# Kernel optimization log

Measured on AMD Instinct MI355X. Metric: run time of the kernel, lower is better.

The kernel has to match this reference:

```python
import jax, jax.numpy as jnp
import numpy as np

D_MODEL = 1024
D_INNER = 2048  # expand * d_model
D_STATE = 16
D_CONV = 4
DT_RANK = 64    # ceil(d_model / 16)
B_SZ, L_SEQ = 2, 1024


def setup_inputs() -> dict:
    key = jax.random.key(0)
    ks = jax.random.split(key, 8)
    s = lambda fan_in: 1.0 / np.sqrt(fan_in)
    x = jax.random.normal(ks[0], (B_SZ, L_SEQ, D_MODEL), dtype=jnp.float32)
    in_proj_w = jax.random.normal(ks[1], (2 * D_INNER, D_MODEL), jnp.float32) * s(D_MODEL)
    conv_w = jax.random.normal(ks[2], (D_INNER, 1, D_CONV), jnp.float32) * s(D_CONV)
    conv_b = jax.random.normal(ks[3], (D_INNER,), jnp.float32) * 0.02
    x_proj_w = jax.random.normal(ks[4], (DT_RANK + 2 * D_STATE, D_INNER), jnp.float32) * s(D_INNER)
    dt_proj_w = jax.random.normal(ks[5], (D_INNER, DT_RANK), jnp.float32) * s(DT_RANK)
    dt_proj_b = jax.random.normal(ks[6], (D_INNER,), jnp.float32) * 0.02
    A_log = jnp.broadcast_to(jnp.log(jnp.arange(1, D_STATE + 1, dtype=jnp.float32)), (D_INNER, D_STATE))
    D_param = jnp.ones((D_INNER,), jnp.float32)
    out_proj_w = jax.random.normal(ks[7], (D_MODEL, D_INNER), jnp.float32) * s(D_INNER)
    return dict(x=x, in_proj_w=in_proj_w, conv_w=conv_w, conv_b=conv_b,
                x_proj_w=x_proj_w, dt_proj_w=dt_proj_w, dt_proj_b=dt_proj_b,
                A_log=A_log, D_param=D_param, out_proj_w=out_proj_w)


def _mamba_forward(x, in_proj_w, conv_w, conv_b, x_proj_w, dt_proj_w, dt_proj_b, A_log, D_param, out_proj_w):
    B, L, _ = x.shape
    # in_proj: (B,L,2*d_inner) -> split into conv branch and gate
    xz = jnp.einsum('bld,ed->ble', x, in_proj_w)
    x_br, z = jnp.split(xz, 2, axis=-1)
    # depthwise causal conv1d (left pad d_conv-1, truncate to L == torch pad+slice)
    xc = jnp.transpose(x_br, (0, 2, 1))  # (B, d_inner, L)
    xc = jax.lax.conv_general_dilated(
        xc, conv_w, window_strides=(1,), padding=[(D_CONV - 1, 0)],
        dimension_numbers=('NCH', 'OIH', 'NCH'), feature_group_count=D_INNER)
    xc = xc + conv_b[None, :, None]
    u = jax.nn.silu(jnp.transpose(xc, (0, 2, 1)))  # (B, L, d_inner) = SSM input
    # input-dependent params
    proj = jnp.einsum('bld,ed->ble', u, x_proj_w)
    delta_raw, B_in, C_in = jnp.split(proj, [DT_RANK, DT_RANK + D_STATE], axis=-1)
    delta = jax.nn.softplus(jnp.einsum('blr,dr->bld', delta_raw, dt_proj_w) + dt_proj_b)
    A = -jnp.exp(A_log)  # (d_inner, d_state)

    def step(h, inp):
        d_t, b_t, c_t, u_t = inp  # (B,d_inner),(B,d_state),(B,d_state),(B,d_inner)
        dA = jnp.exp(d_t[:, :, None] * A)                       # (B,d_inner,d_state)
        h = dA * h + (d_t * u_t)[:, :, None] * b_t[:, None, :]  # ZOH-ish update
        y_t = jnp.einsum('bds,bs->bd', h, c_t) + D_param * u_t
        return h, y_t

    h0 = jnp.zeros((B, D_INNER, D_STATE), dtype=x.dtype)
    inputs = (jnp.swapaxes(delta, 0, 1), jnp.swapaxes(B_in, 0, 1),
              jnp.swapaxes(C_in, 0, 1), jnp.swapaxes(u, 0, 1))
    _, ys = jax.lax.scan(step, h0, inputs)  # (L, B, d_inner)
    y = jnp.swapaxes(ys, 0, 1) * jax.nn.silu(z)
    return jnp.einsum('ble,de->bld', y, out_proj_w)


def reference(x, in_proj_w, conv_w, conv_b, x_proj_w, dt_proj_w, dt_proj_b, A_log, D_param, out_proj_w):
    return _mamba_forward(x, in_proj_w, conv_w, conv_b, x_proj_w, dt_proj_w, dt_proj_b, A_log, D_param, out_proj_w)
```

## Files before the change

kernel.cpp:

```cpp
#include <hip/hip_runtime.h>
#include <hip/hip_bf16.h>

#define D_MODEL 1024
#define D_INNER 2048
#define D_STATE 16
#define D_CONV  4
#define DT_RANK 64
#define B_SZ    2
#define L_SEQ   1024
#define BL      (B_SZ * L_SEQ)
#define NPROJ   (DT_RANK + 2 * D_STATE)

typedef __attribute__((ext_vector_type(8))) short bf16x8;
typedef __attribute__((ext_vector_type(4))) float floatx4;
typedef unsigned short ushort_t;

__device__ __forceinline__ void mfma_bf16(floatx4& acc, bf16x8 a, bf16x8 b) {
    asm volatile("v_mfma_f32_16x16x32_bf16 %0, %1, %2, %0"
                 : "+v"(acc) : "v"(a), "v"(b));
}

__device__ __forceinline__ void cvt_hilo(float f, ushort_t& hi, ushort_t& lo) {
    __hip_bfloat16 h = __float2bfloat16(f);
    hi = *(ushort_t*)&h;
    __hip_bfloat16 l = __float2bfloat16(f - __bfloat162float(h));
    lo = *(ushort_t*)&l;
}

__device__ __forceinline__ void cvt_store4(float4 v, ushort_t* hi, ushort_t* lo) {
    ushort4 h, l;
    cvt_hilo(v.x, h.x, l.x);
    cvt_hilo(v.y, h.y, l.y);
    cvt_hilo(v.z, h.z, l.z);
    cvt_hilo(v.w, h.w, l.w);
    *(ushort4*)hi = h;
    *(ushort4*)lo = l;
}

#define N4_WI 1048576
#define N4_WO 524288
#define N4_X  524288
#define N4_TOT  (N4_WI + N4_WO + N4_X)

__global__ __launch_bounds__(256) void cvt_static(
    const float* __restrict__ wi, ushort_t* wihi, ushort_t* wilo,
    const float* __restrict__ wo, ushort_t* wohi, ushort_t* wolo,
    const float* __restrict__ x,  ushort_t* xhi,  ushort_t* xlo)
{
    int i = blockIdx.x * 256 + threadIdx.x;
    if (i >= N4_TOT) return;
    const float* src; ushort_t *dh, *dl;
    if (i < N4_WI)                 { src = wi; dh = wihi; dl = wilo; }
    else if ((i -= N4_WI) < N4_WO) { src = wo; dh = wohi; dl = wolo; }
    else                           { i -= N4_WO; src = x; dh = xhi; dl = xlo; }
    float4 v = ((const float4*)src)[i];
    cvt_store4(v, dh + i * 4, dl + i * 4);
}

template <int TM, int TN, int KSPLIT>
__global__ __launch_bounds__(256, 2) void gemm_pre(
    const ushort_t* __restrict__ Ahi, const ushort_t* __restrict__ Alo, int lda,
    const ushort_t* __restrict__ Bhi, const ushort_t* __restrict__ Blo, int ldb,
    float* __restrict__ C, int ldc, int K, size_t cslice)
{
    constexpr int LDT = 32;
    constexpr int IT = TM / 32, JT = TN / 32;
    __shared__ __align__(16) ushort_t As[2][TM * LDT];
    __shared__ __align__(16) ushort_t Bs[2][TN * LDT];

    const int tid = threadIdx.x;
    const int bm = blockIdx.y * TM;
    const int bn = blockIdx.x * TN;
    const int kstart = (KSPLIT > 1) ? blockIdx.z * (K / KSPLIT) : 0;
    const int kend   = (KSPLIT > 1) ? kstart + K / KSPLIT : K;

    const int wave = tid >> 6;
    const int lane = tid & 63;
    const int wm = (wave >> 1) * (TM / 2);
    const int wn = (wave & 1) * (TN / 2);
    const int ml = lane & 15;
    const int q  = lane >> 4;

    floatx4 acc[IT][JT];
#pragma unroll
    for (int i = 0; i < IT; ++i)
#pragma unroll
        for (int j = 0; j < JT; ++j) acc[i][j] = (floatx4)0.f;

    for (int k0 = kstart; k0 < kend; k0 += 32) {
        __syncthreads();
#pragma unroll
        for (int ci = 0; ci < TM / 64; ++ci) {
            const int flat = tid + 256 * ci;
            const int r = flat >> 2, c = flat & 3;
            const int p = (c ^ ((r >> 1) & 3)) * 8;
            *(uint4*)&As[0][r * LDT + p] =
                *(const uint4*)(Ahi + (size_t)(bm + r) * lda + k0 + c * 8);
            *(uint4*)&As[1][r * LDT + p] =
                *(const uint4*)(Alo + (size_t)(bm + r) * lda + k0 + c * 8);
        }
#pragma unroll
        for (int ci = 0; ci < TN / 64; ++ci) {
            const int flat = tid + 256 * ci;
            const int r = flat >> 2, c = flat & 3;
            const int p = (c ^ ((r >> 1) & 3)) * 8;
            *(uint4*)&Bs[0][r * LDT + p] =
                *(const uint4*)(Bhi + (size_t)(bn + r) * ldb + k0 + c * 8);
            *(uint4*)&Bs[1][r * LDT + p] =
                *(const uint4*)(Blo + (size_t)(bn + r) * ldb + k0 + c * 8);
        }
        __syncthreads();

        bf16x8 ah[IT], al[IT], bh[JT], bl[JT];
#pragma unroll
        for (int i = 0; i < IT; ++i) {
            const int r = wm + i * 16 + ml;
            const int p = (q ^ ((r >> 1) & 3)) * 8;
            ah[i] = *(const bf16x8*)&As[0][r * LDT + p];
            al[i] = *(const bf16x8*)&As[1][r * LDT + p];
        }
#pragma unroll
        for (int j = 0; j < JT; ++j) {
            const int r = wn + j * 16 + ml;
            const int p = (q ^ ((r >> 1) & 3)) * 8;
            bh[j] = *(const bf16x8*)&Bs[0][r * LDT + p];
            bl[j] = *(const bf16x8*)&Bs[1][r * LDT + p];
        }
#pragma unroll
        for (int i = 0; i < IT; ++i)
#pragma unroll
            for (int j = 0; j < JT; ++j) {
                mfma_bf16(acc[i][j], ah[i], bh[j]);
                mfma_bf16(acc[i][j], ah[i], bl[j]);
                mfma_bf16(acc[i][j], al[i], bh[j]);
            }
    }

    asm volatile("s_nop 7\n\ts_nop 7\n\ts_nop 7" ::: "memory");

    float* Cb = (KSPLIT > 1) ? C + (size_t)blockIdx.z * cslice : C;
#pragma unroll
    for (int i = 0; i < IT; ++i)
#pragma unroll
        for (int j = 0; j < JT; ++j)
#pragma unroll
            for (int r = 0; r < 4; ++r) {
                const int row = bm + wm + i * 16 + q * 4 + r;
                const int col = bn + wn + j * 16 + ml;
                Cb[(size_t)row * ldc + col] = acc[i][j][r];
            }
}

__global__ __launch_bounds__(256) void fold_out(
    const float* __restrict__ s, float* __restrict__ out)
{
    const int i = blockIdx.x * 256 + threadIdx.x;
    const float4* s4 = (const float4*)s;
    constexpr int SL = BL * D_MODEL / 4;
    float4 a = s4[i], b = s4[i + SL], c = s4[i + 2 * SL], d = s4[i + 3 * SL];
    ((float4*)out)[i] = make_float4(a.x + b.x + c.x + d.x,
                                    a.y + b.y + c.y + d.y,
                                    a.z + b.z + c.z + d.z,
                                    a.w + b.w + c.w + d.w);
}

__global__ __launch_bounds__(256) void fold_proj(
    const float* __restrict__ pp, float* __restrict__ proj)
{
    const int i = blockIdx.x * 256 + threadIdx.x;
    constexpr int SL = BL * NPROJ / 4;
    float4 acc = make_float4(0.f, 0.f, 0.f, 0.f);
#pragma unroll
    for (int sp = 0; sp < 16; ++sp) {
        float4 v = ((const float4*)pp)[i + sp * SL];
        acc.x += v.x; acc.y += v.y; acc.z += v.z; acc.w += v.w;
    }
    ((float4*)proj)[i] = acc;
}

__global__ __launch_bounds__(256) void delta_kernel(
    const float* __restrict__ proj,
    const float* __restrict__ Wd,
    const float* __restrict__ bias,
    float* __restrict__ xz)
{
    __shared__ float ps[16][65];
    const int d  = blockIdx.x * 256 + threadIdx.x;
    const int r0 = blockIdx.y * 16;

    {
        const int rr = threadIdx.x >> 4;
        const int cc = (threadIdx.x & 15) * 4;
        float4 v = *(const float4*)(proj + (size_t)(r0 + rr) * NPROJ + cc);
        ps[rr][cc + 0] = v.x; ps[rr][cc + 1] = v.y;
        ps[rr][cc + 2] = v.z; ps[rr][cc + 3] = v.w;
    }
    __syncthreads();

    float w[64];
#pragma unroll
    for (int c4 = 0; c4 < 16; ++c4) {
        float4 v = *(const float4*)(Wd + (size_t)d * 64 + c4 * 4);
        w[c4 * 4 + 0] = v.x; w[c4 * 4 + 1] = v.y;
        w[c4 * 4 + 2] = v.z; w[c4 * 4 + 3] = v.w;
    }
    const float bv = bias[d];

#pragma unroll
    for (int rr = 0; rr < 16; ++rr) {
        float acc = bv;
#pragma unroll
        for (int k = 0; k < 64; ++k) acc += ps[rr][k] * w[k];
        acc = (acc > 20.f) ? acc : log1pf(__expf(acc));
        xz[(size_t)(r0 + rr) * 4096 + d] = acc;
    }
}

#define PKC 128
#define PSC 64

__global__ __launch_bounds__(256) void gemm_proj_conv(
    const float* __restrict__ xz,
    const float* __restrict__ conv_w,
    const float* __restrict__ conv_b,
    const float* __restrict__ Wp,
    float* __restrict__ projp,
    float* __restrict__ u_out)
{
    __shared__ float us[PSC][65];
    __shared__ float wsh[PSC][100];

    const int tid = threadIdx.x;
    const int bm = blockIdx.y * 64;
    const int kbase0 = blockIdx.x * PKC;

    const int tx = tid & 15;
    const int ty = tid >> 4;

    float acc[4][6];
#pragma unroll
    for (int i = 0; i < 4; ++i)
#pragma unroll
        for (int j = 0; j < 6; ++j) acc[i][j] = 0.f;

    for (int sc = 0; sc < PKC / PSC; ++sc) {
        const int kb = kbase0 + sc * PSC;
        __syncthreads();
#pragma unroll
        for (int i = 0; i < 4; ++i) {
            const int flat = tid + 256 * i;
            const int r  = flat >> 4;
            const int kk = (flat & 15) * 4;
            const int k  = kb + kk;
            const int rr = bm + r;
            const int t  = rr & (L_SEQ - 1);
            const float* base = xz + (size_t)rr * 4096 + k;
            float4 x0 = *(const float4*)(base);
            float4 x1 = (t >= 1) ? *(const float4*)(base - 4096)  : make_float4(0,0,0,0);
            float4 x2 = (t >= 2) ? *(const float4*)(base - 8192)  : make_float4(0,0,0,0);
            float4 x3 = (t >= 3) ? *(const float4*)(base - 12288) : make_float4(0,0,0,0);
            float4 cb = *(const float4*)(conv_b + k);
            float4 w0 = ((const float4*)conv_w)[k + 0];
            float4 w1 = ((const float4*)conv_w)[k + 1];
            float4 w2 = ((const float4*)conv_w)[k + 2];
            float4 w3 = ((const float4*)conv_w)[k + 3];
            float4 uo;
            { float a = cb.x + w0.x*x3.x + w0.y*x2.x + w0.z*x1.x + w0.w*x0.x;
              uo.x = a / (1.f + __expf(-a)); }
            { float a = cb.y + w1.x*x3.y + w1.y*x2.y + w1.z*x1.y + w1.w*x0.y;
              uo.y = a / (1.f + __expf(-a)); }
            { float a = cb.z + w2.x*x3.z + w2.y*x2.z + w2.z*x1.z + w2.w*x0.z;
              uo.z = a / (1.f + __expf(-a)); }
            { float a = cb.w + w3.x*x3.w + w3.y*x2.w + w3.z*x1.w + w3.w*x0.w;
              uo.w = a / (1.f + __expf(-a)); }
            us[kk + 0][r] = uo.x;
            us[kk + 1][r] = uo.y;
            us[kk + 2][r] = uo.z;
            us[kk + 3][r] = uo.w;
            *(float4*)(u_out + (size_t)rr * D_INNER + k) = uo;
        }
#pragma unroll
        for (int i = 0; i < 6; ++i) {
            const int flat = tid + 256 * i;
            const int r = flat >> 4;
            const int k4 = flat & 15;
            float4 v = *(const float4*)(Wp + (size_t)r * D_INNER + kb + k4 * 4);
            wsh[k4*4+0][r] = v.x; wsh[k4*4+1][r] = v.y;
            wsh[k4*4+2][r] = v.z; wsh[k4*4+3][r] = v.w;
        }
        __syncthreads();

#pragma unroll 8
        for (int kk = 0; kk < PSC; ++kk) {
            float a[4], b[6];
#pragma unroll
            for (int i = 0; i < 4; ++i) a[i] = us[kk][ty * 4 + i];
#pragma unroll
            for (int j = 0; j < 6; ++j) b[j] = wsh[kk][tx + 16 * j];
#pragma unroll
            for (int i = 0; i < 4; ++i)
#pragma unroll
                for (int j = 0; j < 6; ++j) acc[i][j] += a[i] * b[j];
        }
    }

    float* pb = projp + (size_t)blockIdx.x * (BL * NPROJ);
#pragma unroll
    for (int i = 0; i < 4; ++i)
#pragma unroll
        for (int j = 0; j < 6; ++j)
            pb[(size_t)(bm + ty * 4 + i) * NPROJ + tx + 16 * j] = acc[i][j];
}

template <int CSv>
__global__ __launch_bounds__(256) void scan_phase_a(
    const float* __restrict__ xz,
    const float* __restrict__ u,
    const float* __restrict__ proj,
    const float* __restrict__ A_log,
    float* __restrict__ hloc,
    float* __restrict__ sumd,
    int nc)
{
    const int d = blockIdx.x * 256 + threadIdx.x;
    const int c = blockIdx.y;
    const int b = blockIdx.z;

    float a[D_STATE];
#pragma unroll
    for (int s = 0; s < D_STATE; ++s) a[s] = -__expf(A_log[d * D_STATE + s]);

    float h[D_STATE];
#pragma unroll
    for (int s = 0; s < D_STATE; ++s) h[s] = 0.f;
    float sd = 0.f;

    for (int t = c * CSv; t < (c + 1) * CSv; ++t) {
        const size_t bt = (size_t)b * L_SEQ + t;
        const float dv = xz[bt * (2 * D_INNER) + d];
        const float uv = u[bt * D_INNER + d];
        const float du = dv * uv;
        sd += dv;
        const float* pr = proj + bt * NPROJ;
#pragma unroll
        for (int s = 0; s < D_STATE; ++s)
            h[s] = __expf(dv * a[s]) * h[s] + du * pr[DT_RANK + s];
    }

    const size_t base = ((size_t)(b * nc + c) * D_STATE) * D_INNER + d;
#pragma unroll
    for (int s = 0; s < D_STATE; ++s) hloc[base + (size_t)s * D_INNER] = h[s];
    sumd[(size_t)(b * nc + c) * D_INNER + d] = sd;
}

__global__ __launch_bounds__(256) void scan_phase_b(
    const float* __restrict__ hloc,
    const float* __restrict__ sumd,
    const float* __restrict__ A_log,
    float* __restrict__ carry,
    int nc)
{
    const int g = blockIdx.x * 256 + threadIdx.x;
    const int d = g & (D_INNER - 1);
    const int s = (g >> 11) & (D_STATE - 1);
    const int b = g >> 15;

    const float a_s = -__expf(A_log[d * D_STATE + s]);

    float hc = 0.f;
    carry[((size_t)(b * nc + 0) * D_STATE + s) * D_INNER + d] = 0.f;

    for (int c = 1; c < nc; ++c) {
        const float sd = sumd[(size_t)(b * nc + c - 1) * D_INNER + d];
        const float hl = hloc[((size_t)(b * nc + c - 1) * D_STATE + s) * D_INNER + d];
        hc = __expf(a_s * sd) * hc + hl;
        carry[((size_t)(b * nc + c) * D_STATE + s) * D_INNER + d] = hc;
    }
}

template <int CSv>
__global__ __launch_bounds__(256) void scan_phase_c(
    const float* __restrict__ xz,
    const float* __restrict__ u,
    const float* __restrict__ proj,
    const float* __restrict__ A_log,
    const float* __restrict__ D_param,
    const float* __restrict__ carry,
    ushort_t* __restrict__ Yhi,
    ushort_t* __restrict__ Ylo,
    int nc)
{
    const int d = blockIdx.x * 256 + threadIdx.x;
    const int c = blockIdx.y;
    const int b = blockIdx.z;

    float a[D_STATE];
#pragma unroll
    for (int s = 0; s < D_STATE; ++s) a[s] = -__expf(A_log[d * D_STATE + s]);
    const float Dp = D_param[d];

    float h[D_STATE];
    const size_t cbase = ((size_t)(b * nc + c) * D_STATE) * D_INNER + d;
#pragma unroll
    for (int s = 0; s < D_STATE; ++s) h[s] = carry[cbase + (size_t)s * D_INNER];

    for (int t = c * CSv; t < (c + 1) * CSv; ++t) {
        const size_t bt = (size_t)b * L_SEQ + t;
        const float dv = xz[bt * (2 * D_INNER) + d];
        const float uv = u[bt * D_INNER + d];
        const float du = dv * uv;
        const float* pr = proj + bt * NPROJ;

        float acc = 0.f;
#pragma unroll
        for (int s = 0; s < D_STATE; ++s) {
            h[s] = __expf(dv * a[s]) * h[s] + du * pr[DT_RANK + s];
            acc += h[s] * pr[DT_RANK + D_STATE + s];
        }
        const float yv = acc + Dp * uv;

        const float zv = xz[bt * (2 * D_INNER) + D_INNER + d];
        const float gate = zv / (1.f + __expf(-zv));
        ushort_t hh, ll;
        cvt_hilo(yv * gate, hh, ll);
        Yhi[bt * D_INNER + d] = hh;
        Ylo[bt * D_INNER + d] = ll;
    }
}

extern "C" void kernel_launch(void* const* d_in, const int* in_sizes, int n_in,
                              void* d_out, int out_size, void* d_ws, size_t ws_size,
                              hipStream_t stream)
{
    const float* x         = (const float*)d_in[0];
    const float* in_proj_w = (const float*)d_in[1];
    const float* conv_w    = (const float*)d_in[2];
    const float* conv_b    = (const float*)d_in[3];
    const float* x_proj_w  = (const float*)d_in[4];
    const float* dt_proj_w = (const float*)d_in[5];
    const float* dt_proj_b = (const float*)d_in[6];
    const float* A_log     = (const float*)d_in[7];
    const float* D_param   = (const float*)d_in[8];
    const float* out_proj_w= (const float*)d_in[9];
    float* out = (float*)d_out;

    const size_t fixed =
        (size_t)BL * 4096 * 4 +
        (size_t)BL * 2048 * 4 +
        (size_t)BL * NPROJ * 4 +
        (size_t)(4096 + 2048) * 1024 * 2 * 2;
    const size_t need64 = fixed + (size_t)B_SZ * 64 * D_INNER * 4
                                + (size_t)B_SZ * 64 * D_STATE * D_INNER * 4;
    const int nc = (ws_size >= need64) ? 64 : 32;
    const int cs = L_SEQ / nc;

    float* xz    = (float*)d_ws;
    float* u     = xz    + (size_t)BL * 4096;
    float* proj  = u     + (size_t)BL * 2048;
    float* sumd  = proj  + (size_t)BL * NPROJ;
    float* carry = sumd  + (size_t)B_SZ * nc * D_INNER;
    ushort_t* Wihi = (ushort_t*)(carry + (size_t)B_SZ * nc * D_STATE * D_INNER);
    ushort_t* Wilo = Wihi + (size_t)4096 * 1024;
    ushort_t* Wohi = Wilo + (size_t)4096 * 1024;
    ushort_t* Wolo = Wohi + (size_t)1024 * 2048;
    ushort_t* Xhi  = (ushort_t*)carry;
    ushort_t* Xlo  = Xhi + (size_t)BL * D_MODEL;
    float*    hloc = (float*)Wihi;
    ushort_t* Yhi  = Wihi;
    ushort_t* Ylo  = Wilo;
    float*    projp = (float*)Wihi;
    float*    Cslc  = xz;

    dim3 blk(256);

    cvt_static<<<(N4_TOT + 255) / 256, blk, 0, stream>>>(
        in_proj_w, Wihi, Wilo, out_proj_w, Wohi, Wolo, x, Xhi, Xlo);

    gemm_pre<128, 128, 1><<<dim3(4096 / 128, BL / 128), blk, 0, stream>>>(
        Xhi, Xlo, D_MODEL, Wihi, Wilo, D_MODEL, xz, 2 * D_INNER, D_MODEL, 0);

    gemm_proj_conv<<<dim3(D_INNER / PKC, BL / 64), blk, 0, stream>>>(
        xz, conv_w, conv_b, x_proj_w, projp, u);

    fold_proj<<<(BL * NPROJ / 4) / 256, blk, 0, stream>>>(projp, proj);

    delta_kernel<<<dim3(D_INNER / 256, BL / 16), blk, 0, stream>>>(
        proj, dt_proj_w, dt_proj_b, xz);

    if (cs == 16) {
        scan_phase_a<16><<<dim3(D_INNER / 256, nc, B_SZ), blk, 0, stream>>>(
            xz, u, proj, A_log, hloc, sumd, nc);
    } else {
        scan_phase_a<32><<<dim3(D_INNER / 256, nc, B_SZ), blk, 0, stream>>>(
            xz, u, proj, A_log, hloc, sumd, nc);
    }
    scan_phase_b<<<dim3((B_SZ * D_INNER * D_STATE) / 256), blk, 0, stream>>>(
        hloc, sumd, A_log, carry, nc);
    if (cs == 16) {
        scan_phase_c<16><<<dim3(D_INNER / 256, nc, B_SZ), blk, 0, stream>>>(
            xz, u, proj, A_log, D_param, carry, Yhi, Ylo, nc);
    } else {
        scan_phase_c<32><<<dim3(D_INNER / 256, nc, B_SZ), blk, 0, stream>>>(
            xz, u, proj, A_log, D_param, carry, Yhi, Ylo, nc);
    }

    gemm_pre<128, 128, 4><<<dim3(D_MODEL / 128, BL / 128, 4), blk, 0, stream>>>(
        Yhi, Ylo, D_INNER, Wohi, Wolo, D_INNER, Cslc, D_MODEL, D_INNER,
        (size_t)BL * D_MODEL);
    fold_out<<<(BL * D_MODEL / 4) / 256, blk, 0, stream>>>(Cslc, out);
}
```

Measured before the change: 301.2 us.

## Double-buffer GEMM tiles using direct global-to-LDS loads per wave

The GEMM main loop now double-buffers its shared-memory tiles and fills them with global_load_lds, which copies straight from global memory into LDS without passing through registers. Each wave stages one of the four hi/lo A/B planes. The next K-tile is prefetched while the current one is multiplied, which drops one barrier per iteration and frees the registers that held staged data. In exchange LDS use doubles, which may cut occupancy, and the kernel is now restricted to 128x128 tiles. The direct-to-LDS path also relies on the row-swizzle lane mapping and on the 16-byte load size working correctly on this hardware.

```diff
diff --git a/kernel.cpp b/kernel.cpp
--- a/kernel.cpp
+++ b/kernel.cpp
@@ -63,10 +63,11 @@
     const ushort_t* __restrict__ Bhi, const ushort_t* __restrict__ Blo, int ldb,
     float* __restrict__ C, int ldc, int K, size_t cslice)
 {
+    static_assert(TM == 128 && TN == 128, "stage mapping assumes 128x128");
     constexpr int LDT = 32;
     constexpr int IT = TM / 32, JT = TN / 32;
-    __shared__ __align__(16) ushort_t As[2][TM * LDT];
-    __shared__ __align__(16) ushort_t Bs[2][TN * LDT];
+    __shared__ __align__(16) ushort_t As[2][2][TM * LDT];
+    __shared__ __align__(16) ushort_t Bs[2][2][TN * LDT];
 
     const int tid = threadIdx.x;
     const int bm = blockIdx.y * TM;
@@ -81,50 +82,57 @@
     const int ml = lane & 15;
     const int q  = lane >> 4;
 
+    const ushort_t* gplane = (wave == 0) ? Ahi : (wave == 1) ? Alo
+                           : (wave == 2) ? Bhi : Blo;
+    const int grow0 = (wave < 2) ? bm : bn;
+    const int gld   = (wave < 2) ? lda : ldb;
+    const int rsub  = lane >> 2;
+    const int gg    = ((lane & 3) ^ ((lane >> 3) & 3)) * 8;
+
+    auto stage = [&](int buf, int kc) {
+        ushort_t* lbase = (wave < 2) ? &As[buf][wave & 1][0]
+                                     : &Bs[buf][wave & 1][0];
+#pragma unroll
+        for (int u = 0; u < 8; ++u) {
+            const int R0 = u * 16;
+            const ushort_t* src =
+                gplane + (size_t)(grow0 + R0 + rsub) * gld + kc + gg;
+            __builtin_amdgcn_global_load_lds(
+                (const __attribute__((address_space(1))) unsigned int*)src,
+                (__attribute__((address_space(3))) unsigned int*)(lbase + R0 * LDT),
+                16, 0, 0);
+        }
+    };
+
     floatx4 acc[IT][JT];
 #pragma unroll
     for (int i = 0; i < IT; ++i)
 #pragma unroll
         for (int j = 0; j < JT; ++j) acc[i][j] = (floatx4)0.f;
 
-    for (int k0 = kstart; k0 < kend; k0 += 32) {
-        __syncthreads();
-#pragma unroll
-        for (int ci = 0; ci < TM / 64; ++ci) {
-            const int flat = tid + 256 * ci;
-            const int r = flat >> 2, c = flat & 3;
-            const int p = (c ^ ((r >> 1) & 3)) * 8;
-            *(uint4*)&As[0][r * LDT + p] =
-                *(const uint4*)(Ahi + (size_t)(bm + r) * lda + k0 + c * 8);
-            *(uint4*)&As[1][r * LDT + p] =
-                *(const uint4*)(Alo + (size_t)(bm + r) * lda + k0 + c * 8);
-        }
-#pragma unroll
-        for (int ci = 0; ci < TN / 64; ++ci) {
-            const int flat = tid + 256 * ci;
-            const int r = flat >> 2, c = flat & 3;
-            const int p = (c ^ ((r >> 1) & 3)) * 8;
-            *(uint4*)&Bs[0][r * LDT + p] =
-                *(const uint4*)(Bhi + (size_t)(bn + r) * ldb + k0 + c * 8);
-            *(uint4*)&Bs[1][r * LDT + p] =
-                *(const uint4*)(Blo + (size_t)(bn + r) * ldb + k0 + c * 8);
-        }
-        __syncthreads();
+    const int nt = (kend - kstart) >> 5;
+
+    stage(0, kstart);
+    __syncthreads();
+
+    for (int t = 0; t < nt; ++t) {
+        const int buf = t & 1;
+        if (t + 1 < nt) stage(buf ^ 1, kstart + ((t + 1) << 5));
 
         bf16x8 ah[IT], al[IT], bh[JT], bl[JT];
 #pragma unroll
         for (int i = 0; i < IT; ++i) {
             const int r = wm + i * 16 + ml;
             const int p = (q ^ ((r >> 1) & 3)) * 8;
-            ah[i] = *(const bf16x8*)&As[0][r * LDT + p];
-            al[i] = *(const bf16x8*)&As[1][r * LDT + p];
+            ah[i] = *(const bf16x8*)&As[buf][0][r * LDT + p];
+            al[i] = *(const bf16x8*)&As[buf][1][r * LDT + p];
         }
 #pragma unroll
         for (int j = 0; j < JT; ++j) {
             const int r = wn + j * 16 + ml;
             const int p = (q ^ ((r >> 1) & 3)) * 8;
-            bh[j] = *(const bf16x8*)&Bs[0][r * LDT + p];
-            bl[j] = *(const bf16x8*)&Bs[1][r * LDT + p];
+            bh[j] = *(const bf16x8*)&Bs[buf][0][r * LDT + p];
+            bl[j] = *(const bf16x8*)&Bs[buf][1][r * LDT + p];
         }
 #pragma unroll
         for (int i = 0; i < IT; ++i)
@@ -134,6 +142,8 @@
                 mfma_bf16(acc[i][j], ah[i], bl[j]);
                 mfma_bf16(acc[i][j], al[i], bh[j]);
             }
+
+        __syncthreads();
     }
 
     asm volatile("s_nop 7\n\ts_nop 7\n\ts_nop 7" ::: "memory");
```

After: 296.9 us. About the same (-1.4%).
